# Performance work log

Hardware: AMD Instinct MI355X
Metric: run time of the kernel (lower is better)

Reference implementation:

```python
import jax, jax.numpy as jnp
import numpy as np

D = 512   # Nsites: single-particle Hilbert space dimension
N = 128   # Nparticles
TINY = 1e-30


def setup_inputs() -> dict:
    key = jax.random.key(0)
    k1, k2 = jax.random.split(key)
    # Orthonormal orbitals (mirrors reortho_orbitals: QR of a random matrix)
    A = jax.random.normal(k1, (D, D), dtype=jnp.float32)
    Q, _ = jnp.linalg.qr(A)
    P = Q[:, :N]                                   # (D, N) orthonormal columns
    u = jax.random.uniform(k2, (N,), dtype=jnp.float32)  # inverse-CDF draws, one per particle
    return {"P": P, "u": u}


def _sample(P, u):
    """Ordered componentwise sampling from the Slater determinant.

    Uses the identity that Ksites is always a contiguous range [0..i], so the
    determinant ratios -det(G[0:i+1]-diag(occ+e_i))/det(G[0:x_{k-1}+1]-diag(occ))
    reduce to running products of Schur-complement pivots s_j = G_jj - b^T Xinv b
    of the leading block of (G - diag(occ)).  A single O(D) scan maintains the
    (padded) inverse of that leading block via rank-1 bordered-inverse updates,
    replacing the per-step np.ix_/vstack/det kernel launches of the original.
    """
    dt = P.dtype
    G = jnp.eye(D, dtype=dt) - P @ P.T             # (D, D), symmetric projection complement
    idxs = jnp.arange(D)

    def step(carry, i):
        Xinv, ratio, cumul, k = carry
        b = jnp.where(idxs < i, G[:, i], 0.0)      # border column, masked to leading block
        v = Xinv @ b                               # Xinv is zero-padded beyond processed block
        s = G[i, i] - b @ v                        # Schur pivot (site i unoccupied)
        last_allowed = D - N + k                   # xmax - 1 for particle k
        active = (k < N) & (i <= last_allowed)
        # cond prob particle k sits at site i: -(s-1) * prod of unoccupied pivots since x_{k-1}
        p = jnp.where(active, -(s - 1.0) * ratio, 0.0)
        u_k = u[jnp.clip(k, 0, N - 1)]
        occupy = active & ((cumul + p >= u_k) | (i == last_allowed))  # inverse-CDF; force at support end
        pivot = jnp.where(occupy, s - 1.0, s)
        pivot = jnp.where(jnp.abs(pivot) < TINY, TINY, pivot)
        # bordered inverse update: [[X,b],[b,d]]^-1 via outer(vext,vext)/pivot
        vext = jnp.where(idxs == i, -1.0, v)
        Xinv = Xinv + jnp.outer(vext, vext) / pivot
        ratio = jnp.where(occupy, 1.0, jnp.where(active, ratio * s, ratio))
        cumul = jnp.where(occupy, 0.0, cumul + p)
        k = k + occupy.astype(jnp.int32)
        return (Xinv, ratio, cumul, k), (p, k - occupy.astype(jnp.int32), occupy)

    init = (jnp.zeros((D, D), dtype=dt), jnp.asarray(1.0, dt), jnp.asarray(0.0, dt),
            jnp.asarray(0, jnp.int32))
    _, (p_rec, k_rec, occ_rec) = jax.lax.scan(step, init, idxs)

    krow = jnp.where(k_rec < N, k_rec, N)          # out-of-range rows dropped
    cond_probs = jnp.zeros((N, D), dtype=dt).at[krow, idxs].set(p_rec, mode='drop')
    return cond_probs, occ_rec


def reference(P, u):
    cond_probs, occ = _sample(P, u)
    positions = jnp.nonzero(occ, size=N, fill_value=-1)[0]  # ordered sampled sites
    return cond_probs, positions
```

## Files before the change

### kernel.cpp

```cpp
#include <hip/hip_runtime.h>


#define DD 512
#define NN 128
#define NTHREADS 512
#define BB 16
#define NBLK (DD / BB)

typedef float v2f __attribute__((ext_vector_type(2)));

__device__ __forceinline__ float lane_bcast(float v, int l) {
  return __int_as_float(__builtin_amdgcn_readlane(__float_as_int(v), l));
}

__device__ __forceinline__ void pk_fma_vs(v2f& acc, v2f a, v2f bs) {
  asm("v_pk_fma_f32 %0, %1, %2, %0" : "+v"(acc) : "v"(a), "s"(bs));
}
__device__ __forceinline__ v2f pk_mul_vs(v2f a, v2f bs) {
  v2f d;
  asm("v_pk_mul_f32 %0, %1, %2" : "=v"(d) : "v"(a), "s"(bs));
  return d;
}

__device__ __forceinline__ float wave_reduce_add64(float sd) {
#if __has_builtin(__builtin_amdgcn_permlane32_swap)
  {
    unsigned xi = __float_as_uint(sd);
    auto r = __builtin_amdgcn_permlane32_swap(xi, xi, false, false);
    sd = __uint_as_float(r[0]) + __uint_as_float(r[1]);
  }
#else
  sd += __shfl_xor(sd, 32, 64);
#endif
#if __has_builtin(__builtin_amdgcn_permlane16_swap)
  {
    unsigned xi = __float_as_uint(sd);
    auto r = __builtin_amdgcn_permlane16_swap(xi, xi, false, false);
    sd = __uint_as_float(r[0]) + __uint_as_float(r[1]);
  }
#else
  sd += __shfl_xor(sd, 16, 64);
#endif
  sd += __int_as_float(
      __builtin_amdgcn_update_dpp(0, __float_as_int(sd), 0x128, 0xF, 0xF, true));
  sd += __int_as_float(
      __builtin_amdgcn_ds_swizzle(__float_as_int(sd), 0x101F));
  sd += __int_as_float(
      __builtin_amdgcn_update_dpp(0, __float_as_int(sd), 0x4E, 0xF, 0xF, true));
  sd += __int_as_float(
      __builtin_amdgcn_update_dpp(0, __float_as_int(sd), 0xB1, 0xF, 0xF, true));
  return sd;
}

__global__ __launch_bounds__(NTHREADS) void slater_scan_kernel(
    const float* __restrict__ P, const float* __restrict__ u,
    float* __restrict__ out) {
  const int tid   = threadIdx.x;
  const int wave  = tid >> 6;
  const int lane  = tid & 63;
  const int c0    = wave << 4;
  const int rbase = c0 & 63;
  const bool lowhalf = (wave < 4);

  __shared__ __align__(16) float part[8][64][36];
  __shared__ __align__(16) float Vld[128][20];
  __shared__ __align__(16) float Cld[16][20];

  for (int j = tid; j < NN * DD; j += NTHREADS) out[j] = 0.0f;

  const float ur0 = u[lane];
  const float ur1 = u[64 + lane];

  v2f A2r0[8], A2r1[8];
#pragma unroll
  for (int jp = 0; jp < 8; ++jp) {
    A2r0[jp] = (v2f){(lane == c0 + 2 * jp) ? 1.0f : 0.0f,
                     (lane == c0 + 2 * jp + 1) ? 1.0f : 0.0f};
    A2r1[jp] = (v2f){(lane + 64 == c0 + 2 * jp) ? 1.0f : 0.0f,
                     (lane + 64 == c0 + 2 * jp + 1) ? 1.0f : 0.0f};
  }

  float ratio = 1.0f, cumul = 0.0f;
  int k = 0;

  __syncthreads();

  for (int blk = 0; blk < NBLK; ++blk) {
    const int i0 = blk * BB;
    const int c0u = __builtin_amdgcn_readfirstlane(c0);
    const float* Pu = P + i0 * NN + c0u;

    const int tr = i0 + 2 * wave;
    const float pt0l = P[tr * NN + lane];
    const float pt0h = P[tr * NN + 64 + lane];
    const float pt1l = P[tr * NN + NN + lane];
    const float pt1h = P[tr * NN + NN + 64 + lane];

    float pa0[16], pa1[16];
#pragma unroll
    for (int t = 0; t < 16; ++t) {
      const v2f* pr2 = (const v2f*)(Pu + t * NN);
      v2f a0 = pk_mul_vs(A2r0[0], pr2[0]);
      v2f a1 = pk_mul_vs(A2r1[0], pr2[0]);
#pragma unroll
      for (int jp = 1; jp < 8; ++jp) {
        const v2f sp = pr2[jp];
        pk_fma_vs(a0, A2r0[jp], sp);
        pk_fma_vs(a1, A2r1[jp], sp);
      }
      pa0[t] = a0.x + a0.y;
      pa1[t] = a1.x + a1.y;
    }
    {
      float4* myp = (float4*)&part[wave][lane][0];
      myp[0] = make_float4(pa0[0],  pa0[1],  pa0[2],  pa0[3]);
      myp[1] = make_float4(pa0[4],  pa0[5],  pa0[6],  pa0[7]);
      myp[2] = make_float4(pa0[8],  pa0[9],  pa0[10], pa0[11]);
      myp[3] = make_float4(pa0[12], pa0[13], pa0[14], pa0[15]);
      myp[4] = make_float4(pa1[0],  pa1[1],  pa1[2],  pa1[3]);
      myp[5] = make_float4(pa1[4],  pa1[5],  pa1[6],  pa1[7]);
      myp[6] = make_float4(pa1[8],  pa1[9],  pa1[10], pa1[11]);
      myp[7] = make_float4(pa1[12], pa1[13], pa1[14], pa1[15]);
    }
    __syncthreads();

    {
      const int r  = tid >> 2;
      const int qd = tid & 3;
      const int rl = r & 63;
      const int rh = (r >> 6) << 4;
      float s0 = 0.f, s1 = 0.f, s2 = 0.f, s3 = 0.f;
#pragma unroll
      for (int v = 0; v < 8; ++v) {
        const float4 x = *(const float4*)&part[v][rl][rh + 4 * qd];
        s0 += x.x; s1 += x.y; s2 += x.z; s3 += x.w;
      }
      *(float4*)&Vld[r][4 * qd] = make_float4(s0, s1, s2, s3);
    }
    __syncthreads();

    float W0[16], W1[16];
#pragma unroll
    for (int qd = 0; qd < 4; ++qd) {
      const float4 x = *(const float4*)&Vld[lane][4 * qd];
      W0[4 * qd + 0] = x.x; W0[4 * qd + 1] = x.y;
      W0[4 * qd + 2] = x.z; W0[4 * qd + 3] = x.w;
      const float4 y = *(const float4*)&Vld[lane + 64][4 * qd];
      W1[4 * qd + 0] = y.x; W1[4 * qd + 1] = y.y;
      W1[4 * qd + 2] = y.z; W1[4 * qd + 3] = y.w;
    }

    {
      float cr0[16], cr1[16];
#pragma unroll
      for (int mm = 0; mm < 16; ++mm) {
        cr0[mm] = wave_reduce_add64(fmaf(pt0l, W0[mm], pt0h * W1[mm]));
        cr1[mm] = wave_reduce_add64(fmaf(pt1l, W0[mm], pt1h * W1[mm]));
      }
      if (lane == 0) {
        float4* cp0 = (float4*)&Cld[2 * wave][0];
        cp0[0] = make_float4(cr0[0],  cr0[1],  cr0[2],  cr0[3]);
        cp0[1] = make_float4(cr0[4],  cr0[5],  cr0[6],  cr0[7]);
        cp0[2] = make_float4(cr0[8],  cr0[9],  cr0[10], cr0[11]);
        cp0[3] = make_float4(cr0[12], cr0[13], cr0[14], cr0[15]);
        float4* cp1 = (float4*)&Cld[2 * wave + 1][0];
        cp1[0] = make_float4(cr1[0],  cr1[1],  cr1[2],  cr1[3]);
        cp1[1] = make_float4(cr1[4],  cr1[5],  cr1[6],  cr1[7]);
        cp1[2] = make_float4(cr1[8],  cr1[9],  cr1[10], cr1[11]);
        cp1[3] = make_float4(cr1[12], cr1[13], cr1[14], cr1[15]);
      }
    }
    __syncthreads();

    const int m = lane & 15;
    float Cc[16];
#pragma unroll
    for (int t = 0; t < 16; ++t) Cc[t] = Cld[t][m];
    float qdiag = Cld[m][m];
    float Dreg[16], SD[16], SW0[16], SW1[16];
    bool done = false;
#pragma unroll
    for (int t = 0; t < 16; ++t) {
      const float s = 1.0f - lane_bcast(qdiag, t);
      const int i = i0 + t;
      const int last_allowed = DD - NN + k;
      const bool active = (k < NN) && (i <= last_allowed);
      const float pr = active ? (-(s - 1.0f) * ratio) : 0.0f;
      const int kidx = (k < NN) ? k : (NN - 1);
      const float uk_l = lane_bcast(ur0, kidx & 63);
      const float uk_h = lane_bcast(ur1, kidx & 63);
      const float uk = (kidx < 64) ? uk_l : uk_h;
      const bool occupy = active && ((cumul + pr >= uk) || (i == last_allowed));
      float pivot = occupy ? (s - 1.0f) : s;
      pivot = (fabsf(pivot) < 1e-30f) ? 1e-30f : pivot;
      const float invp = 1.0f / pivot;

      if (tid == 0) {
        if (k < NN) out[k * DD + i] = pr;
        if (occupy) out[NN * DD + k] = (float)i;
      }

      ratio = occupy ? 1.0f : (active ? ratio * s : ratio);
      cumul = occupy ? 0.0f : (cumul + pr);
      k += occupy ? 1 : 0;
      if (k == NN) { done = true; break; }

      float d = Cc[t];
#pragma unroll
      for (int j = 0; j < t; ++j) {
        const float djt = lane_bcast(Dreg[j], t);
        d     = fmaf(djt, SD[j],  d);
        W0[t] = fmaf(djt, SW0[j], W0[t]);
        W1[t] = fmaf(djt, SW1[j], W1[t]);
      }
      Dreg[t] = d;
      SD[t]   = d * invp;
      SW0[t]  = W0[t] * invp;
      SW1[t]  = W1[t] * invp;
      qdiag   = fmaf(d, SD[t], qdiag);
    }
    if (done) return;

    {
      auto upd = [&](const float (&Wh)[16]) {
#pragma unroll
        for (int t = 0; t < 16; ++t) {
          const v2f w0d = {SW0[t], SW0[t]};
          const v2f w1d = {SW1[t], SW1[t]};
#pragma unroll
          for (int jp = 0; jp < 8; ++jp) {
            const v2f wc2 = {lane_bcast(Wh[t], rbase + 2 * jp),
                             lane_bcast(Wh[t], rbase + 2 * jp + 1)};
            pk_fma_vs(A2r0[jp], w0d, wc2);
            pk_fma_vs(A2r1[jp], w1d, wc2);
          }
        }
      };
      if (lowhalf) upd(W0); else upd(W1);
    }
  }
}

extern "C" void kernel_launch(void* const* d_in, const int* in_sizes, int n_in,
                              void* d_out, int out_size, void* d_ws,
                              size_t ws_size, hipStream_t stream) {
  const float* P = (const float*)d_in[0];
  const float* u = (const float*)d_in[1];
  float* out = (float*)d_out;
  hipLaunchKernelGGL(slater_scan_kernel, dim3(1), dim3(NTHREADS), 0, stream,
                     P, u, out);
}
```

Before: 484.4 us.

## Double-buffer P tiles in LDS and pack W updates into v_pk ops

Each block's 16 rows of P are now staged into a double-buffered LDS array, with the next block prefetched into registers and written during the current block. This replaces the per-iteration global/scalar loads of P. The W0/W1 arrays are merged into packed v2f pairs so the triangular update uses v_pk_fma. The Vld staging array is transposed to produce those pairs, and the partial-sum reduction uses packed adds. The change costs extra LDS space and more register pressure from holding the prefetch.

```diff
diff --git a/kernel.cpp b/kernel.cpp
--- a/kernel.cpp
+++ b/kernel.cpp
@@ -12,14 +12,19 @@
 __device__ __forceinline__ float lane_bcast(float v, int l) {
   return __int_as_float(__builtin_amdgcn_readlane(__float_as_int(v), l));
 }
-
+__device__ __forceinline__ void pk_fma_vv(v2f& acc, v2f a, v2f b) {
+  asm("v_pk_fma_f32 %0, %1, %2, %0" : "+v"(acc) : "v"(a), "v"(b));
+}
 __device__ __forceinline__ void pk_fma_vs(v2f& acc, v2f a, v2f bs) {
   asm("v_pk_fma_f32 %0, %1, %2, %0" : "+v"(acc) : "v"(a), "s"(bs));
 }
-__device__ __forceinline__ v2f pk_mul_vs(v2f a, v2f bs) {
+__device__ __forceinline__ v2f pk_mul_vv(v2f a, v2f b) {
   v2f d;
-  asm("v_pk_mul_f32 %0, %1, %2" : "=v"(d) : "v"(a), "s"(bs));
+  asm("v_pk_mul_f32 %0, %1, %2" : "=v"(d) : "v"(a), "v"(b));
   return d;
+}
+__device__ __forceinline__ void pk_add_vv(v2f& acc, v2f a) {
+  asm("v_pk_add_f32 %0, %1, %0" : "+v"(acc) : "v"(a));
 }
 
 __device__ __forceinline__ float wave_reduce_add64(float sd) {
@@ -63,13 +68,18 @@
   const bool lowhalf = (wave < 4);
 
   __shared__ __align__(16) float part[8][64][36];
-  __shared__ __align__(16) float Vld[128][20];
+  __shared__ __align__(16) float VldT[16][129];
   __shared__ __align__(16) float Cld[16][20];
+  __shared__ __align__(16) float Pst[2][BB][NN];
 
   for (int j = tid; j < NN * DD; j += NTHREADS) out[j] = 0.0f;
 
   const float ur0 = u[lane];
   const float ur1 = u[64 + lane];
+
+  const int sr = tid >> 5;
+  const int sc = (tid & 31) << 2;
+  *(float4*)&Pst[0][sr][sc] = *(const float4*)&P[sr * NN + sc];
 
   v2f A2r0[8], A2r1[8];
 #pragma unroll
@@ -86,28 +96,39 @@
   __syncthreads();
 
   for (int blk = 0; blk < NBLK; ++blk) {
-    const int i0 = blk * BB;
-    const int c0u = __builtin_amdgcn_readfirstlane(c0);
-    const float* Pu = P + i0 * NN + c0u;
-
-    const int tr = i0 + 2 * wave;
-    const float pt0l = P[tr * NN + lane];
-    const float pt0h = P[tr * NN + 64 + lane];
-    const float pt1l = P[tr * NN + NN + lane];
-    const float pt1h = P[tr * NN + NN + 64 + lane];
+    const int i0  = blk * BB;
+    const int buf = blk & 1;
+
+    float4 stg;
+    const bool do_stage = (blk + 1 < NBLK);
+    if (do_stage) stg = *(const float4*)&P[(i0 + BB + sr) * NN + sc];
+
+    const int t2 = 2 * wave;
+    const float pt0l = Pst[buf][t2][lane];
+    const float pt0h = Pst[buf][t2][64 + lane];
+    const float pt1l = Pst[buf][t2 + 1][lane];
+    const float pt1h = Pst[buf][t2 + 1][64 + lane];
 
     float pa0[16], pa1[16];
 #pragma unroll
     for (int t = 0; t < 16; ++t) {
-      const v2f* pr2 = (const v2f*)(Pu + t * NN);
-      v2f a0 = pk_mul_vs(A2r0[0], pr2[0]);
-      v2f a1 = pk_mul_vs(A2r1[0], pr2[0]);
-#pragma unroll
-      for (int jp = 1; jp < 8; ++jp) {
-        const v2f sp = pr2[jp];
-        pk_fma_vs(a0, A2r0[jp], sp);
-        pk_fma_vs(a1, A2r1[jp], sp);
-      }
+      const float4 q0 = *(const float4*)&Pst[buf][t][c0];
+      const float4 q1 = *(const float4*)&Pst[buf][t][c0 + 4];
+      const float4 q2 = *(const float4*)&Pst[buf][t][c0 + 8];
+      const float4 q3 = *(const float4*)&Pst[buf][t][c0 + 12];
+      const v2f pp0 = {q0.x, q0.y}, pp1 = {q0.z, q0.w};
+      const v2f pp2 = {q1.x, q1.y}, pp3 = {q1.z, q1.w};
+      const v2f pp4 = {q2.x, q2.y}, pp5 = {q2.z, q2.w};
+      const v2f pp6 = {q3.x, q3.y}, pp7 = {q3.z, q3.w};
+      v2f a0 = pk_mul_vv(A2r0[0], pp0);
+      v2f a1 = pk_mul_vv(A2r1[0], pp0);
+      pk_fma_vv(a0, A2r0[1], pp1); pk_fma_vv(a1, A2r1[1], pp1);
+      pk_fma_vv(a0, A2r0[2], pp2); pk_fma_vv(a1, A2r1[2], pp2);
+      pk_fma_vv(a0, A2r0[3], pp3); pk_fma_vv(a1, A2r1[3], pp3);
+      pk_fma_vv(a0, A2r0[4], pp4); pk_fma_vv(a1, A2r1[4], pp4);
+      pk_fma_vv(a0, A2r0[5], pp5); pk_fma_vv(a1, A2r1[5], pp5);
+      pk_fma_vv(a0, A2r0[6], pp6); pk_fma_vv(a1, A2r1[6], pp6);
+      pk_fma_vv(a0, A2r0[7], pp7); pk_fma_vv(a1, A2r1[7], pp7);
       pa0[t] = a0.x + a0.y;
       pa1[t] = a1.x + a1.y;
     }
@@ -122,6 +143,7 @@
       myp[6] = make_float4(pa1[8],  pa1[9],  pa1[10], pa1[11]);
       myp[7] = make_float4(pa1[12], pa1[13], pa1[14], pa1[15]);
     }
+    if (do_stage) *(float4*)&Pst[buf ^ 1][sr][sc] = stg;
     __syncthreads();
 
     {
@@ -129,41 +151,39 @@
       const int qd = tid & 3;
       const int rl = r & 63;
       const int rh = (r >> 6) << 4;
-      float s0 = 0.f, s1 = 0.f, s2 = 0.f, s3 = 0.f;
+      v2f s01 = {0.0f, 0.0f}, s23 = {0.0f, 0.0f};
 #pragma unroll
       for (int v = 0; v < 8; ++v) {
         const float4 x = *(const float4*)&part[v][rl][rh + 4 * qd];
-        s0 += x.x; s1 += x.y; s2 += x.z; s3 += x.w;
-      }
-      *(float4*)&Vld[r][4 * qd] = make_float4(s0, s1, s2, s3);
+        pk_add_vv(s01, (v2f){x.x, x.y});
+        pk_add_vv(s23, (v2f){x.z, x.w});
+      }
+      VldT[4 * qd + 0][r] = s01.x;
+      VldT[4 * qd + 1][r] = s01.y;
+      VldT[4 * qd + 2][r] = s23.x;
+      VldT[4 * qd + 3][r] = s23.y;
     }
     __syncthreads();
 
-    float W0[16], W1[16];
-#pragma unroll
-    for (int qd = 0; qd < 4; ++qd) {
-      const float4 x = *(const float4*)&Vld[lane][4 * qd];
-      W0[4 * qd + 0] = x.x; W0[4 * qd + 1] = x.y;
-      W0[4 * qd + 2] = x.z; W0[4 * qd + 3] = x.w;
-      const float4 y = *(const float4*)&Vld[lane + 64][4 * qd];
-      W1[4 * qd + 0] = y.x; W1[4 * qd + 1] = y.y;
-      W1[4 * qd + 2] = y.z; W1[4 * qd + 3] = y.w;
-    }
+    v2f Wp[16];
+#pragma unroll
+    for (int m2 = 0; m2 < 16; ++m2)
+      Wp[m2] = (v2f){VldT[m2][lane], VldT[m2][lane + 64]};
 
     {
       float cr0[16], cr1[16];
 #pragma unroll
       for (int mm = 0; mm < 16; ++mm) {
-        cr0[mm] = wave_reduce_add64(fmaf(pt0l, W0[mm], pt0h * W1[mm]));
-        cr1[mm] = wave_reduce_add64(fmaf(pt1l, W0[mm], pt1h * W1[mm]));
+        cr0[mm] = wave_reduce_add64(fmaf(pt0l, Wp[mm].x, pt0h * Wp[mm].y));
+        cr1[mm] = wave_reduce_add64(fmaf(pt1l, Wp[mm].x, pt1h * Wp[mm].y));
       }
       if (lane == 0) {
-        float4* cp0 = (float4*)&Cld[2 * wave][0];
+        float4* cp0 = (float4*)&Cld[t2][0];
         cp0[0] = make_float4(cr0[0],  cr0[1],  cr0[2],  cr0[3]);
         cp0[1] = make_float4(cr0[4],  cr0[5],  cr0[6],  cr0[7]);
         cp0[2] = make_float4(cr0[8],  cr0[9],  cr0[10], cr0[11]);
         cp0[3] = make_float4(cr0[12], cr0[13], cr0[14], cr0[15]);
-        float4* cp1 = (float4*)&Cld[2 * wave + 1][0];
+        float4* cp1 = (float4*)&Cld[t2 + 1][0];
         cp1[0] = make_float4(cr1[0],  cr1[1],  cr1[2],  cr1[3]);
         cp1[1] = make_float4(cr1[4],  cr1[5],  cr1[6],  cr1[7]);
         cp1[2] = make_float4(cr1[8],  cr1[9],  cr1[10], cr1[11]);
@@ -177,7 +197,8 @@
 #pragma unroll
     for (int t = 0; t < 16; ++t) Cc[t] = Cld[t][m];
     float qdiag = Cld[m][m];
-    float Dreg[16], SD[16], SW0[16], SW1[16];
+    float Dreg[16], SD[16];
+    v2f SWp[16];
     bool done = false;
 #pragma unroll
     for (int t = 0; t < 16; ++t) {
@@ -209,34 +230,33 @@
 #pragma unroll
       for (int j = 0; j < t; ++j) {
         const float djt = lane_bcast(Dreg[j], t);
-        d     = fmaf(djt, SD[j],  d);
-        W0[t] = fmaf(djt, SW0[j], W0[t]);
-        W1[t] = fmaf(djt, SW1[j], W1[t]);
+        d = fmaf(djt, SD[j], d);
+        pk_fma_vs(Wp[t], SWp[j], (v2f){djt, djt});
       }
       Dreg[t] = d;
       SD[t]   = d * invp;
-      SW0[t]  = W0[t] * invp;
-      SW1[t]  = W1[t] * invp;
+      SWp[t]  = pk_mul_vv(Wp[t], (v2f){invp, invp});
       qdiag   = fmaf(d, SD[t], qdiag);
     }
     if (done) return;
 
     {
-      auto upd = [&](const float (&Wh)[16]) {
+      auto upd = [&](bool low) {
 #pragma unroll
         for (int t = 0; t < 16; ++t) {
-          const v2f w0d = {SW0[t], SW0[t]};
-          const v2f w1d = {SW1[t], SW1[t]};
+          const v2f w0d = {SWp[t].x, SWp[t].x};
+          const v2f w1d = {SWp[t].y, SWp[t].y};
+          const float wsrc = low ? Wp[t].x : Wp[t].y;
 #pragma unroll
           for (int jp = 0; jp < 8; ++jp) {
-            const v2f wc2 = {lane_bcast(Wh[t], rbase + 2 * jp),
-                             lane_bcast(Wh[t], rbase + 2 * jp + 1)};
+            const v2f wc2 = {lane_bcast(wsrc, rbase + 2 * jp),
+                             lane_bcast(wsrc, rbase + 2 * jp + 1)};
             pk_fma_vs(A2r0[jp], w0d, wc2);
             pk_fma_vs(A2r1[jp], w1d, wc2);
           }
         }
       };
-      if (lowhalf) upd(W0); else upd(W1);
+      if (lowhalf) upd(true); else upd(false);
     }
   }
 }
```

After: 464.2 us. -4.2%, faster.
